# Kernel tuning notes

Measured on AMD Instinct MI355X. Metric: run time of the kernel, lower is better.

## Reference

```python
import jax, jax.numpy as jnp
import numpy as np

OBJ = 6
N_OBJS = 16
ACT = 32
HID = 128


def _mlp(x, W1, b1, W2, b2, W3, b3):
    # RoboticsMLP with layer_sizes=[128,128]: Linear->ReLU->Linear->ReLU->Linear
    h = jax.nn.relu(x @ W1 + b1)
    h = jax.nn.relu(h @ W2 + b2)
    return h @ W3 + b3


def setup_inputs() -> dict:
    key = jax.random.key(0)
    ks = jax.random.split(key, 16)
    B = 4096
    s = lambda fan_in: 1.0 / np.sqrt(fan_in)
    u_in = OBJ + ACT          # 38
    b_in = 2 * OBJ + ACT      # 44
    return {
        "config": jax.random.normal(ks[0], (B, N_OBJS * OBJ), dtype=jnp.float32),
        "action": jax.random.normal(ks[1], (B, ACT), dtype=jnp.float32),
        "uW1": jax.random.normal(ks[2], (u_in, HID), dtype=jnp.float32) * s(u_in),
        "ub1": jnp.zeros((HID,), jnp.float32),
        "uW2": jax.random.normal(ks[3], (HID, HID), dtype=jnp.float32) * s(HID),
        "ub2": jnp.zeros((HID,), jnp.float32),
        "uW3": jax.random.normal(ks[4], (HID, OBJ), dtype=jnp.float32) * s(HID),
        "ub3": jnp.zeros((OBJ,), jnp.float32),
        "bW1": jax.random.normal(ks[5], (b_in, HID), dtype=jnp.float32) * s(b_in),
        "bb1": jnp.zeros((HID,), jnp.float32),
        "bW2": jax.random.normal(ks[6], (HID, HID), dtype=jnp.float32) * s(HID),
        "bb2": jnp.zeros((HID,), jnp.float32),
        "bW3": jax.random.normal(ks[7], (HID, OBJ), dtype=jnp.float32) * s(HID),
        "bb3": jnp.zeros((OBJ,), jnp.float32),
    }


def reference(config, action, uW1, ub1, uW2, ub2, uW3, ub3,
              bW1, bb1, bW2, bb2, bW3, bb3):
    B = config.shape[0]
    objs = config.reshape(B, N_OBJS, OBJ)                       # [B, N, 6]

    # Unary: per-object MLP on [obj, action]
    act_b = jnp.broadcast_to(action[:, None, :], (B, N_OBJS, ACT))
    u_in = jnp.concatenate([objs, act_b], axis=-1)              # [B, N, 6+A]
    u_out = _mlp(u_in, uW1, ub1, uW2, ub2, uW3, ub3)            # [B, N, 6]

    # Binary: all ordered pairs (i, j), i != j: [obj_i, obj_j, action]
    oi = jnp.broadcast_to(objs[:, :, None, :], (B, N_OBJS, N_OBJS, OBJ))
    oj = jnp.broadcast_to(objs[:, None, :, :], (B, N_OBJS, N_OBJS, OBJ))
    act_p = jnp.broadcast_to(action[:, None, None, :], (B, N_OBJS, N_OBJS, ACT))
    b_in = jnp.concatenate([oi, oj, act_p], axis=-1)            # [B, N, N, 12+A]
    b_out = _mlp(b_in, bW1, bb1, bW2, bb2, bW3, bb3)            # [B, N, N, 6]

    # zero out diagonal (i == j skipped in original) then sum over j
    mask = (1.0 - jnp.eye(N_OBJS, dtype=b_out.dtype))[None, :, :, None]
    b_sum = (b_out * mask).sum(axis=2)                          # [B, N, 6]

    out = objs + u_out + b_sum
    return out.reshape(B, N_OBJS * OBJ)
```

## Files before the change

kernel.cpp:

```cpp
#include <hip/hip_runtime.h>

typedef short bf16x8 __attribute__((ext_vector_type(8)));
typedef float f32x4 __attribute__((ext_vector_type(4)));

__device__ __forceinline__ unsigned short f2bf(float f) {
    unsigned int u = __float_as_uint(f);
    unsigned int r = u + 0x7FFFu + ((u >> 16) & 1u);
    return (unsigned short)(r >> 16);
}

__device__ __forceinline__ unsigned pkbf(float a, float b) {
    unsigned r;
    asm volatile("v_cvt_pk_bf16_f32 %0, %1, %2" : "=v"(r) : "v"(a), "v"(b));
    return r;
}

__global__ __launch_bounds__(256) void prep_all(
        const float* __restrict__ uW1, const float* __restrict__ uW2, const float* __restrict__ uW3,
        const float* __restrict__ bW1, const float* __restrict__ bW2, const float* __restrict__ bW3,
        unsigned short* __restrict__ ws) {
    int idx = blockIdx.x * 256 + threadIdx.x;
    const float* W; int Ksrc, Nsrc, ntsh; unsigned short* dst; int li;
    if (idx < 8192)       { W = uW1; Ksrc = 38;  Nsrc = 128; ntsh = 10; dst = ws;         li = idx; }
    else if (idx < 16384) { W = bW1; Ksrc = 44;  Nsrc = 128; ntsh = 10; dst = ws + 8192;  li = idx - 8192; }
    else if (idx < 32768) { W = uW2; Ksrc = 128; Nsrc = 128; ntsh = 11; dst = ws + 16384; li = idx - 16384; }
    else if (idx < 49152) { W = bW2; Ksrc = 128; Nsrc = 128; ntsh = 11; dst = ws + 32768; li = idx - 32768; }
    else if (idx < 51200) { W = uW3; Ksrc = 128; Nsrc = 6;   ntsh = 11; dst = ws + 49152; li = idx - 49152; }
    else if (idx < 53248) { W = bW3; Ksrc = 128; Nsrc = 6;   ntsh = 11; dst = ws + 51200; li = idx - 51200; }
    else return;
    int e  = li & 7;
    int l  = (li >> 3) & 63;
    int KS = (ntsh == 10) ? 2 : 4;
    int ks = (li >> 9) & (KS - 1);
    int nt = li >> ntsh;
    int k  = ks * 32 + (l >> 4) * 8 + e;
    int n  = nt * 16 + (l & 15);
    float v = (k < Ksrc && n < Nsrc) ? W[k * Nsrc + n] : 0.0f;
    dst[li] = f2bf(v);
}

__global__ __launch_bounds__(256, 3) void unary_kernel(
        const float* __restrict__ config, const float* __restrict__ action,
        const unsigned short* __restrict__ W1f, const float* __restrict__ b1,
        const unsigned short* __restrict__ W2f, const float* __restrict__ b2,
        const unsigned short* __restrict__ W3f, const float* __restrict__ b3,
        float* __restrict__ out) {
    __shared__ __align__(16) unsigned char smem[4 * 8192];
    const int tid = threadIdx.x;
    const int w = tid >> 6;
    const int l = tid & 63;
    const int g = l >> 4;
    const int c = l & 15;
    unsigned char* buf = smem + w * 8192;

    {
        const int rowL = l >> 1;
        const int kh   = l & 1;
        const int sw   = (rowL & 7) << 4;
        const int base = rowL * 128 + kh * 64;
        const int rg = blockIdx.x * 128 + w * 32 + rowL;
        const int b = rg >> 4;
        const int i = rg & 15;
        const float* cbr = config + b * 96 + i * 6;
        const float* ab  = action + b * 32;
        if (kh == 0) {
            float ov[6];
            { const float2 t0 = *(const float2*)(cbr);
              const float2 t1 = *(const float2*)(cbr + 2);
              const float2 t2 = *(const float2*)(cbr + 4);
              ov[0]=t0.x; ov[1]=t0.y; ov[2]=t1.x; ov[3]=t1.y; ov[4]=t2.x; ov[5]=t2.y; }
            float av[26];
            #pragma unroll
            for (int q = 0; q < 6; ++q) {
                const float4 t = *(const float4*)(ab + 4 * q);
                av[4*q]=t.x; av[4*q+1]=t.y; av[4*q+2]=t.z; av[4*q+3]=t.w;
            }
            { const float2 t = *(const float2*)(ab + 24); av[24]=t.x; av[25]=t.y; }
            #pragma unroll
            for (int ch = 0; ch < 4; ++ch) {
                float x[8];
                #pragma unroll
                for (int t8 = 0; t8 < 8; ++t8) {
                    const int k = ch * 8 + t8;
                    x[t8] = (k < 6) ? ov[k] : av[k - 6];
                }
                union { unsigned uu[4]; bf16x8 v; } U;
                U.uu[0] = pkbf(x[0], x[1]); U.uu[1] = pkbf(x[2], x[3]);
                U.uu[2] = pkbf(x[4], x[5]); U.uu[3] = pkbf(x[6], x[7]);
                *(bf16x8*)(buf + ((base + ch * 16) ^ sw)) = U.v;
            }
        } else {
            float av2[6];
            { const float2 t = *(const float2*)(ab + 26); av2[0]=t.x; av2[1]=t.y; }
            { const float4 t = *(const float4*)(ab + 28); av2[2]=t.x; av2[3]=t.y; av2[4]=t.z; av2[5]=t.w; }
            {
                union { unsigned uu[4]; bf16x8 v; } U;
                U.uu[0] = pkbf(av2[0], av2[1]); U.uu[1] = pkbf(av2[2], av2[3]);
                U.uu[2] = pkbf(av2[4], av2[5]); U.uu[3] = 0u;
                *(bf16x8*)(buf + ((base + 0) ^ sw)) = U.v;
            }
            const bf16x8 z = {0,0,0,0,0,0,0,0};
            *(bf16x8*)(buf + ((base + 16) ^ sw)) = z;
            *(bf16x8*)(buf + ((base + 32) ^ sw)) = z;
            *(bf16x8*)(buf + ((base + 48) ^ sw)) = z;
        }
    }
    __syncthreads();

    const f32x4 zero4 = {0.f, 0.f, 0.f, 0.f};

    bf16x8 xf[2][2];
    #pragma unroll
    for (int mt = 0; mt < 2; ++mt)
        #pragma unroll
        for (int ks = 0; ks < 2; ++ks) {
            const int row = mt * 16 + c;
            xf[mt][ks] = *(const bf16x8*)(buf + ((row * 128 + ks * 64 + g * 16) ^ ((c & 7) << 4)));
        }

    #pragma unroll
    for (int nh = 0; nh < 2; ++nh) {
        f32x4 acc[2][4];
        #pragma unroll
        for (int mt = 0; mt < 2; ++mt)
            #pragma unroll
            for (int ntl = 0; ntl < 4; ++ntl) acc[mt][ntl] = zero4;
        #pragma unroll
        for (int ntl = 0; ntl < 4; ++ntl) {
            const int nt = nh * 4 + ntl;
            #pragma unroll
            for (int ks = 0; ks < 2; ++ks) {
                const bf16x8 bfr = *(const bf16x8*)(W1f + ((nt * 2 + ks) * 64 + l) * 8);
                #pragma unroll
                for (int mt = 0; mt < 2; ++mt)
                    acc[mt][ntl] = __builtin_amdgcn_mfma_f32_16x16x32_bf16(xf[mt][ks], bfr, acc[mt][ntl], 0, 0, 0);
            }
        }
        #pragma unroll
        for (int ntl = 0; ntl < 4; ++ntl) {
            const int col = (nh * 4 + ntl) * 16 + c;
            const float bias = b1[col];
            #pragma unroll
            for (int mt = 0; mt < 2; ++mt)
                #pragma unroll
                for (int r = 0; r < 4; ++r) {
                    const int row = mt * 16 + g * 4 + r;
                    const float hv = fmaxf(acc[mt][ntl][r] + bias, 0.f);
                    *(unsigned short*)(buf + ((row * 256 + col * 2) ^ ((row & 7) << 4))) = f2bf(hv);
                }
        }
    }
    __syncthreads();

    bf16x8 hf[2][4];
    #pragma unroll
    for (int mt = 0; mt < 2; ++mt)
        #pragma unroll
        for (int ks = 0; ks < 4; ++ks) {
            const int row = mt * 16 + c;
            hf[mt][ks] = *(const bf16x8*)(buf + ((row * 256 + ks * 64 + g * 16) ^ ((c & 7) << 4)));
        }

    #pragma unroll
    for (int nh = 0; nh < 2; ++nh) {
        f32x4 acc[2][4];
        #pragma unroll
        for (int mt = 0; mt < 2; ++mt)
            #pragma unroll
            for (int ntl = 0; ntl < 4; ++ntl) acc[mt][ntl] = zero4;
        #pragma unroll
        for (int ntl = 0; ntl < 4; ++ntl) {
            const int nt = nh * 4 + ntl;
            #pragma unroll
            for (int ks = 0; ks < 4; ++ks) {
                const bf16x8 bfr = *(const bf16x8*)(W2f + ((nt * 4 + ks) * 64 + l) * 8);
                #pragma unroll
                for (int mt = 0; mt < 2; ++mt)
                    acc[mt][ntl] = __builtin_amdgcn_mfma_f32_16x16x32_bf16(hf[mt][ks], bfr, acc[mt][ntl], 0, 0, 0);
            }
        }
        #pragma unroll
        for (int ntl = 0; ntl < 4; ++ntl) {
            const int col = (nh * 4 + ntl) * 16 + c;
            const float bias = b2[col];
            #pragma unroll
            for (int mt = 0; mt < 2; ++mt)
                #pragma unroll
                for (int r = 0; r < 4; ++r) {
                    const int row = mt * 16 + g * 4 + r;
                    const float hv = fmaxf(acc[mt][ntl][r] + bias, 0.f);
                    *(unsigned short*)(buf + ((row * 256 + col * 2) ^ ((row & 7) << 4))) = f2bf(hv);
                }
        }
    }
    __syncthreads();

    bf16x8 h2f[2][4];
    #pragma unroll
    for (int mt = 0; mt < 2; ++mt)
        #pragma unroll
        for (int ks = 0; ks < 4; ++ks) {
            const int row = mt * 16 + c;
            h2f[mt][ks] = *(const bf16x8*)(buf + ((row * 256 + ks * 64 + g * 16) ^ ((c & 7) << 4)));
        }

    f32x4 acc3[2];
    acc3[0] = zero4; acc3[1] = zero4;
    #pragma unroll
    for (int ks = 0; ks < 4; ++ks) {
        const bf16x8 bfr = *(const bf16x8*)(W3f + (ks * 64 + l) * 8);
        #pragma unroll
        for (int mt = 0; mt < 2; ++mt)
            acc3[mt] = __builtin_amdgcn_mfma_f32_16x16x32_bf16(h2f[mt][ks], bfr, acc3[mt], 0, 0, 0);
    }

    const int rgbase = blockIdx.x * 128 + w * 32;
    const float b3v = (c < 6) ? b3[c] : 0.f;
    #pragma unroll
    for (int mt = 0; mt < 2; ++mt)
        #pragma unroll
        for (int r = 0; r < 4; ++r) {
            const int rg = rgbase + mt * 16 + g * 4 + r;
            const int b = rg >> 4, i = rg & 15;
            if (c < 6) {
                const int idx = b * 96 + i * 6 + c;
                out[idx] = acc3[mt][r] + b3v + config[idx];
            }
        }
}

__global__ __launch_bounds__(256, 5) void binary_kernel(
        const float* __restrict__ config, const float* __restrict__ action,
        const unsigned short* __restrict__ W1f, const float* __restrict__ b1,
        const unsigned short* __restrict__ W2f, const float* __restrict__ b2,
        const unsigned short* __restrict__ W3f, const float* __restrict__ b3,
        float* __restrict__ out) {
    __shared__ __align__(16) unsigned char PQs[12288];
    __shared__ __align__(16) unsigned char UNs[8192];

    unsigned char* Ts = UNs;
    const int tid = threadIdx.x;
    const int w = tid >> 6, l = tid & 63, g = l >> 4, c = l & 15;
    const int b = blockIdx.x >> 1, h = blockIdx.x & 1;
    const float* cb = config + b * 96;
    const float* ab = action + b * 32;
    const f32x4 zero4 = {0.f, 0.f, 0.f, 0.f};

    {
        const int p  = tid >> 3;
        const int k0 = (tid & 7) * 8;
        union { unsigned short us[8]; bf16x8 v; } u;
        #pragma unroll
        for (int e = 0; e < 8; ++e) {
            const int k = k0 + e;
            float x = 0.f;
            if (p < 8) {
                if (k < 6) x = cb[(8 * h + p) * 6 + k];
                else if (k >= 12 && k < 44) x = ab[k - 12];
            } else if (p >= 16) {
                if (k >= 6 && k < 12) x = cb[(p - 16) * 6 + (k - 6)];
            }
            u.us[e] = f2bf(x);
        }
        *(bf16x8*)(Ts + ((p * 128 + k0 * 2) ^ ((p & 7) << 4))) = u.v;
    }
    __syncthreads();

    {
        bf16x8 tfr[2][2];
        #pragma unroll
        for (int nt = 0; nt < 2; ++nt)
            #pragma unroll
            for (int ks = 0; ks < 2; ++ks)
                tfr[nt][ks] = *(const bf16x8*)(Ts + (((c + 16 * nt) * 128 + 64 * ks + 16 * g) ^ ((c & 7) << 4)));
        f32x4 acc1[2][2];
        acc1[0][0] = zero4; acc1[0][1] = zero4; acc1[1][0] = zero4; acc1[1][1] = zero4;
        #pragma unroll
        for (int mt1 = 0; mt1 < 2; ++mt1) {
            #pragma unroll
            for (int ks = 0; ks < 2; ++ks) {
                const bf16x8 wfr = *(const bf16x8*)(W1f + (((2 * w + mt1) * 2 + ks) * 64 + l) * 8);
                acc1[mt1][0] = __builtin_amdgcn_mfma_f32_16x16x32_bf16(wfr, tfr[0][ks], acc1[mt1][0], 0, 0, 0);
                acc1[mt1][1] = __builtin_amdgcn_mfma_f32_16x16x32_bf16(wfr, tfr[1][ks], acc1[mt1][1], 0, 0, 0);
            }
        }
        #pragma unroll
        for (int mt1 = 0; mt1 < 2; ++mt1) {
            const f32x4 bv = *(const f32x4*)(b1 + 32 * w + 16 * mt1 + 4 * g);
            acc1[mt1][0] = acc1[mt1][0] + bv;
            const int fb = (32 * w + 16 * mt1 + 4 * g) * 4;
            if (c < 8) {
                float2 v0; v0.x = acc1[mt1][0][0]; v0.y = acc1[mt1][0][1];
                float2 v1; v1.x = acc1[mt1][0][2]; v1.y = acc1[mt1][0][3];
                *(float2*)(PQs + ((c * 512 + fb)     ^ ((c & 7) << 4))) = v0;
                *(float2*)(PQs + ((c * 512 + fb + 8) ^ ((c & 7) << 4))) = v1;
            }
            {
                const int row = 8 + c;
                float2 v0; v0.x = acc1[mt1][1][0]; v0.y = acc1[mt1][1][1];
                float2 v1; v1.x = acc1[mt1][1][2]; v1.y = acc1[mt1][1][3];
                *(float2*)(PQs + ((row * 512 + fb)     ^ ((c & 7) << 4))) = v0;
                *(float2*)(PQs + ((row * 512 + fb + 8) ^ ((c & 7) << 4))) = v1;
            }
        }
    }
    __syncthreads();

    const int i0 = h * 8 + 2 * w;
    bf16x8 h1f[2][4];
    #pragma unroll
    for (int nt = 0; nt < 2; ++nt) {
        const int ip = 2 * w + nt;
        #pragma unroll
        for (int ks = 0; ks < 4; ++ks) {
            const int kb = (32 * ks + 8 * g) * 4;
            const f32x4 p0 = *(const f32x4*)(PQs + ((ip * 512 + kb) ^ ((ip & 7) << 4)));
            const f32x4 p1 = *(const f32x4*)(PQs + ((ip * 512 + kb + 16) ^ ((ip & 7) << 4)));
            const f32x4 q0 = *(const f32x4*)(PQs + (((8 + c) * 512 + kb) ^ ((c & 7) << 4)));
            const f32x4 q1 = *(const f32x4*)(PQs + (((8 + c) * 512 + kb + 16) ^ ((c & 7) << 4)));
            union { unsigned u[4]; bf16x8 v; } un;
            un.u[0] = pkbf(fmaxf(p0[0] + q0[0], 0.f), fmaxf(p0[1] + q0[1], 0.f));
            un.u[1] = pkbf(fmaxf(p0[2] + q0[2], 0.f), fmaxf(p0[3] + q0[3], 0.f));
            un.u[2] = pkbf(fmaxf(p1[0] + q1[0], 0.f), fmaxf(p1[1] + q1[1], 0.f));
            un.u[3] = pkbf(fmaxf(p1[2] + q1[2], 0.f), fmaxf(p1[3] + q1[3], 0.f));
            h1f[nt][ks] = un.v;
        }
    }

    unsigned char* Ck = UNs + w * 2048;
    f32x4 acc3[2];
    acc3[0] = zero4; acc3[1] = zero4;
    #pragma unroll 1
    for (int ks = 0; ks < 4; ++ks) {
        f32x4 a2[2][2];
        a2[0][0] = zero4; a2[0][1] = zero4; a2[1][0] = zero4; a2[1][1] = zero4;
        #pragma unroll
        for (int ksp = 0; ksp < 4; ++ksp) {
            #pragma unroll
            for (int mt1 = 0; mt1 < 2; ++mt1) {
                const bf16x8 wf = *(const bf16x8*)(W2f + (((2 * ks + mt1) * 4 + ksp) * 64 + l) * 8);
                a2[mt1][0] = __builtin_amdgcn_mfma_f32_16x16x32_bf16(wf, h1f[0][ksp], a2[mt1][0], 0, 0, 0);
                a2[mt1][1] = __builtin_amdgcn_mfma_f32_16x16x32_bf16(wf, h1f[1][ksp], a2[mt1][1], 0, 0, 0);
            }
        }
        #pragma unroll
        for (int mt1 = 0; mt1 < 2; ++mt1) {
            const f32x4 bv = *(const f32x4*)(b2 + 32 * ks + 16 * mt1 + 4 * g);
            #pragma unroll
            for (int nt = 0; nt < 2; ++nt) {
                const int p = c + 16 * nt;
                uint2 pk2;
                pk2.x = pkbf(fmaxf(a2[mt1][nt][0] + bv[0], 0.f), fmaxf(a2[mt1][nt][1] + bv[1], 0.f));
                pk2.y = pkbf(fmaxf(a2[mt1][nt][2] + bv[2], 0.f), fmaxf(a2[mt1][nt][3] + bv[3], 0.f));
                *(uint2*)(Ck + ((p * 64 + 32 * mt1 + 8 * g) ^ (((p >> 1) & 3) << 4))) = pk2;
            }
        }
        const bf16x8 w3 = *(const bf16x8*)(W3f + (ks * 64 + l) * 8);
        #pragma unroll
        for (int nt = 0; nt < 2; ++nt) {
            const int p = c + 16 * nt;
            const bf16x8 ha = *(const bf16x8*)(Ck + ((p * 64 + 16 * g) ^ (((p >> 1) & 3) << 4)));
            acc3[nt] = __builtin_amdgcn_mfma_f32_16x16x32_bf16(ha, w3, acc3[nt], 0, 0, 0);
        }
    }

    const float b3v = (c < 6) ? b3[c] : 0.f;
    #pragma unroll
    for (int nt = 0; nt < 2; ++nt) {
        const int i = i0 + nt;
        float s = 0.f;
        #pragma unroll
        for (int r = 0; r < 4; ++r) {
            const int j = 4 * g + r;
            if (j != i) s += acc3[nt][r] + b3v;
        }
        s += __shfl_xor(s, 16, 64);
        s += __shfl_xor(s, 32, 64);
        if (g == 0 && c < 6) out[b * 96 + i * 6 + c] += s;
    }
}

extern "C" void kernel_launch(void* const* d_in, const int* in_sizes, int n_in,
                              void* d_out, int out_size, void* d_ws, size_t ws_size,
                              hipStream_t stream) {
    const float* config = (const float*)d_in[0];
    const float* action = (const float*)d_in[1];
    const float* uW1 = (const float*)d_in[2];
    const float* ub1 = (const float*)d_in[3];
    const float* uW2 = (const float*)d_in[4];
    const float* ub2 = (const float*)d_in[5];
    const float* uW3 = (const float*)d_in[6];
    const float* ub3 = (const float*)d_in[7];
    const float* bW1 = (const float*)d_in[8];
    const float* bb1 = (const float*)d_in[9];
    const float* bW2 = (const float*)d_in[10];
    const float* bb2 = (const float*)d_in[11];
    const float* bW3 = (const float*)d_in[12];
    const float* bb3 = (const float*)d_in[13];
    float* out = (float*)d_out;

    unsigned short* ws   = (unsigned short*)d_ws;
    unsigned short* uW1f = ws;
    unsigned short* bW1f = ws + 8192;
    unsigned short* uW2f = ws + 16384;
    unsigned short* bW2f = ws + 32768;
    unsigned short* uW3f = ws + 49152;
    unsigned short* bW3f = ws + 51200;

    prep_all<<<208, 256, 0, stream>>>(uW1, uW2, uW3, bW1, bW2, bW3, ws);
    unary_kernel<<<512, 256, 0, stream>>>(config, action, uW1f, ub1, uW2f, ub2, uW3f, ub3, out);
    binary_kernel<<<8192, 256, 0, stream>>>(config, action, bW1f, bb1, bW2f, bb2, bW3f, bb3, out);
}
```

Measured before the change: 164.3 us.

## Build binary layer-1 operands in registers and drop a barrier and zero MFMAs

```diff
diff --git a/kernel.cpp b/kernel.cpp
--- a/kernel.cpp
+++ b/kernel.cpp
@@ -229,16 +229,15 @@
         }
 }
 
-__global__ __launch_bounds__(256, 5) void binary_kernel(
+__global__ __launch_bounds__(256, 4) void binary_kernel(
         const float* __restrict__ config, const float* __restrict__ action,
         const unsigned short* __restrict__ W1f, const float* __restrict__ b1,
         const unsigned short* __restrict__ W2f, const float* __restrict__ b2,
         const unsigned short* __restrict__ W3f, const float* __restrict__ b3,
         float* __restrict__ out) {
     __shared__ __align__(16) unsigned char PQs[12288];
-    __shared__ __align__(16) unsigned char UNs[8192];
-
-    unsigned char* Ts = UNs;
+    __shared__ __align__(16) unsigned char Cks[8192];
+
     const int tid = threadIdx.x;
     const int w = tid >> 6, l = tid & 63, g = l >> 4, c = l & 15;
     const int b = blockIdx.x >> 1, h = blockIdx.x & 1;
@@ -246,43 +245,57 @@
     const float* ab = action + b * 32;
     const f32x4 zero4 = {0.f, 0.f, 0.f, 0.f};
 
+    bf16x8 tP0, tP1, tQ0;
     {
-        const int p  = tid >> 3;
-        const int k0 = (tid & 7) * 8;
-        union { unsigned short us[8]; bf16x8 v; } u;
-        #pragma unroll
-        for (int e = 0; e < 8; ++e) {
-            const int k = k0 + e;
-            float x = 0.f;
-            if (p < 8) {
-                if (k < 6) x = cb[(8 * h + p) * 6 + k];
-                else if (k >= 12 && k < 44) x = ab[k - 12];
-            } else if (p >= 16) {
-                if (k >= 6 && k < 12) x = cb[(p - 16) * 6 + (k - 6)];
-            }
-            u.us[e] = f2bf(x);
-        }
-        *(bf16x8*)(Ts + ((p * 128 + k0 * 2) ^ ((p & 7) << 4))) = u.v;
-    }
-    __syncthreads();
+        const bf16x8 z8 = {0,0,0,0,0,0,0,0};
+        tP0 = z8; tP1 = z8; tQ0 = z8;
+        union { unsigned u[4]; bf16x8 v; } U;
+        if (g == 0) {
+            const float* obp = cb + (8 * h + (c & 7)) * 6;
+            const float2 a0 = *(const float2*)obp, a1 = *(const float2*)(obp + 2), a2 = *(const float2*)(obp + 4);
+            U.u[0] = pkbf(a0.x, a0.y); U.u[1] = pkbf(a1.x, a1.y); U.u[2] = pkbf(a2.x, a2.y); U.u[3] = 0u;
+            tP0 = U.v;
+            const float4 b0 = *(const float4*)(ab + 20), b1v = *(const float4*)(ab + 24);
+            U.u[0] = pkbf(b0.x, b0.y); U.u[1] = pkbf(b0.z, b0.w);
+            U.u[2] = pkbf(b1v.x, b1v.y); U.u[3] = pkbf(b1v.z, b1v.w);
+            tP1 = U.v;
+            const float2 q0 = *(const float2*)(cb + c * 6);
+            U.u[0] = 0u; U.u[1] = 0u; U.u[2] = 0u; U.u[3] = pkbf(q0.x, q0.y);
+            tQ0 = U.v;
+        } else if (g == 1) {
+            const float4 b0 = *(const float4*)(ab + 0);
+            U.u[0] = 0u; U.u[1] = 0u; U.u[2] = pkbf(b0.x, b0.y); U.u[3] = pkbf(b0.z, b0.w);
+            tP0 = U.v;
+            const float4 b1v = *(const float4*)(ab + 28);
+            U.u[0] = pkbf(b1v.x, b1v.y); U.u[1] = pkbf(b1v.z, b1v.w); U.u[2] = 0u; U.u[3] = 0u;
+            tP1 = U.v;
+            const float* obq = cb + c * 6;
+            const float2 q1 = *(const float2*)(obq + 2), q2 = *(const float2*)(obq + 4);
+            U.u[0] = pkbf(q1.x, q1.y); U.u[1] = pkbf(q2.x, q2.y); U.u[2] = 0u; U.u[3] = 0u;
+            tQ0 = U.v;
+        } else if (g == 2) {
+            const float4 b0 = *(const float4*)(ab + 4), b1v = *(const float4*)(ab + 8);
+            U.u[0] = pkbf(b0.x, b0.y); U.u[1] = pkbf(b0.z, b0.w);
+            U.u[2] = pkbf(b1v.x, b1v.y); U.u[3] = pkbf(b1v.z, b1v.w);
+            tP0 = U.v;
+        } else {
+            const float4 b0 = *(const float4*)(ab + 12), b1v = *(const float4*)(ab + 16);
+            U.u[0] = pkbf(b0.x, b0.y); U.u[1] = pkbf(b0.z, b0.w);
+            U.u[2] = pkbf(b1v.x, b1v.y); U.u[3] = pkbf(b1v.z, b1v.w);
+            tP0 = U.v;
+        }
+    }
 
     {
-        bf16x8 tfr[2][2];
-        #pragma unroll
-        for (int nt = 0; nt < 2; ++nt)
-            #pragma unroll
-            for (int ks = 0; ks < 2; ++ks)
-                tfr[nt][ks] = *(const bf16x8*)(Ts + (((c + 16 * nt) * 128 + 64 * ks + 16 * g) ^ ((c & 7) << 4)));
         f32x4 acc1[2][2];
         acc1[0][0] = zero4; acc1[0][1] = zero4; acc1[1][0] = zero4; acc1[1][1] = zero4;
         #pragma unroll
         for (int mt1 = 0; mt1 < 2; ++mt1) {
-            #pragma unroll
-            for (int ks = 0; ks < 2; ++ks) {
-                const bf16x8 wfr = *(const bf16x8*)(W1f + (((2 * w + mt1) * 2 + ks) * 64 + l) * 8);
-                acc1[mt1][0] = __builtin_amdgcn_mfma_f32_16x16x32_bf16(wfr, tfr[0][ks], acc1[mt1][0], 0, 0, 0);
-                acc1[mt1][1] = __builtin_amdgcn_mfma_f32_16x16x32_bf16(wfr, tfr[1][ks], acc1[mt1][1], 0, 0, 0);
-            }
+            const bf16x8 wf0 = *(const bf16x8*)(W1f + (((2 * w + mt1) * 2 + 0) * 64 + l) * 8);
+            const bf16x8 wf1 = *(const bf16x8*)(W1f + (((2 * w + mt1) * 2 + 1) * 64 + l) * 8);
+            acc1[mt1][0] = __builtin_amdgcn_mfma_f32_16x16x32_bf16(wf0, tP0, acc1[mt1][0], 0, 0, 0);
+            acc1[mt1][0] = __builtin_amdgcn_mfma_f32_16x16x32_bf16(wf1, tP1, acc1[mt1][0], 0, 0, 0);
+            acc1[mt1][1] = __builtin_amdgcn_mfma_f32_16x16x32_bf16(wf0, tQ0, acc1[mt1][1], 0, 0, 0);
         }
         #pragma unroll
         for (int mt1 = 0; mt1 < 2; ++mt1) {
@@ -309,15 +322,15 @@
     const int i0 = h * 8 + 2 * w;
     bf16x8 h1f[2][4];
     #pragma unroll
-    for (int nt = 0; nt < 2; ++nt) {
-        const int ip = 2 * w + nt;
-        #pragma unroll
-        for (int ks = 0; ks < 4; ++ks) {
-            const int kb = (32 * ks + 8 * g) * 4;
+    for (int ks = 0; ks < 4; ++ks) {
+        const int kb = (32 * ks + 8 * g) * 4;
+        const f32x4 q0 = *(const f32x4*)(PQs + (((8 + c) * 512 + kb) ^ ((c & 7) << 4)));
+        const f32x4 q1 = *(const f32x4*)(PQs + (((8 + c) * 512 + kb + 16) ^ ((c & 7) << 4)));
+        #pragma unroll
+        for (int nt = 0; nt < 2; ++nt) {
+            const int ip = 2 * w + nt;
             const f32x4 p0 = *(const f32x4*)(PQs + ((ip * 512 + kb) ^ ((ip & 7) << 4)));
             const f32x4 p1 = *(const f32x4*)(PQs + ((ip * 512 + kb + 16) ^ ((ip & 7) << 4)));
-            const f32x4 q0 = *(const f32x4*)(PQs + (((8 + c) * 512 + kb) ^ ((c & 7) << 4)));
-            const f32x4 q1 = *(const f32x4*)(PQs + (((8 + c) * 512 + kb + 16) ^ ((c & 7) << 4)));
             union { unsigned u[4]; bf16x8 v; } un;
             un.u[0] = pkbf(fmaxf(p0[0] + q0[0], 0.f), fmaxf(p0[1] + q0[1], 0.f));
             un.u[1] = pkbf(fmaxf(p0[2] + q0[2], 0.f), fmaxf(p0[3] + q0[3], 0.f));
@@ -327,10 +340,10 @@
         }
     }
 
-    unsigned char* Ck = UNs + w * 2048;
+    unsigned char* Ck = Cks + w * 2048;
     f32x4 acc3[2];
     acc3[0] = zero4; acc3[1] = zero4;
-    #pragma unroll 1
+    #pragma unroll
     for (int ks = 0; ks < 4; ++ks) {
         f32x4 a2[2][2];
         a2[0][0] = zero4; a2[0][1] = zero4; a2[1][0] = zero4; a2[1][1] = zero4;
@@ -352,14 +365,14 @@
                 uint2 pk2;
                 pk2.x = pkbf(fmaxf(a2[mt1][nt][0] + bv[0], 0.f), fmaxf(a2[mt1][nt][1] + bv[1], 0.f));
                 pk2.y = pkbf(fmaxf(a2[mt1][nt][2] + bv[2], 0.f), fmaxf(a2[mt1][nt][3] + bv[3], 0.f));
-                *(uint2*)(Ck + ((p * 64 + 32 * mt1 + 8 * g) ^ (((p >> 1) & 3) << 4))) = pk2;
+                *(uint2*)(Ck + ((p * 64 + 32 * mt1 + 8 * g) ^ ((p & 7) << 4))) = pk2;
             }
         }
         const bf16x8 w3 = *(const bf16x8*)(W3f + (ks * 64 + l) * 8);
         #pragma unroll
         for (int nt = 0; nt < 2; ++nt) {
             const int p = c + 16 * nt;
-            const bf16x8 ha = *(const bf16x8*)(Ck + ((p * 64 + 16 * g) ^ (((p >> 1) & 3) << 4)));
+            const bf16x8 ha = *(const bf16x8*)(Ck + ((p * 64 + 16 * g) ^ ((p & 7) << 4)));
             acc3[nt] = __builtin_amdgcn_mfma_f32_16x16x32_bf16(ha, w3, acc3[nt], 0, 0, 0);
         }
     }
```

New measurement: 162.3 us. Within noise of the previous version (-1.2%).
